# Performance work log

Hardware: AMD Instinct MI355X
Metric: run time of the kernel (lower is better)

The kernel has to match this reference:

```python
import jax, jax.numpy as jnp
import numpy as np

# ---- constants matching init_kwargs ----
N_ELEMENT = 8
N_LINES = 32
LINES_PER_ELEM = 4  # n_line_group_each_element = [4]*8
MINIBATCH = 512
SAMPLE_N = 1024
SAMPLE_CM = 0.01
PROBE_I0 = 100000.0
SIGNAL_ATT = 1.0
DET_SOLID_ANGLE_RATIO = 0.05
N_VOXEL_MB = MINIBATCH * SAMPLE_N


def setup_inputs() -> dict:
    key = jax.random.key(0)
    k1, k2, k3, k4 = jax.random.split(key, 4)
    xp = jax.random.uniform(k1, (N_ELEMENT, MINIBATCH, SAMPLE_N), dtype=jnp.float32)
    mu_probe = jax.random.uniform(k2, (N_ELEMENT,), dtype=jnp.float32)
    fl_unit = jax.random.uniform(k3, (N_LINES,), dtype=jnp.float32)
    SA_theta = jax.random.uniform(k4, (N_LINES, N_VOXEL_MB), dtype=jnp.float32)
    return {"xp": xp, "mu_probe": mu_probe, "fl_unit": fl_unit, "SA_theta": SA_theta}


def reference(xp, mu_probe, fl_unit, SA_theta):
    # xp: (E, B, N) concentration minibatch, theta==0 so rotation is skipped.
    conc = xp  # (E, B, N)

    # Probe attenuation: per-element LAC, prefix-sum along beam axis,
    # zero-padded at entry face, summed over elements.
    lac = conc * mu_probe[:, None, None]                     # (E, B, N)
    lac_acc = jnp.cumsum(lac, axis=-1)                       # (E, B, N)
    zeros_col = jnp.zeros((N_ELEMENT, MINIBATCH, 1), dtype=conc.dtype)
    lac_acc = jnp.concatenate([zeros_col, lac_acc], axis=-1) # (E, B, N+1)
    att_exponent_acc_map = jnp.sum(lac_acc, axis=0) * (SAMPLE_CM / SAMPLE_N)  # (B, N+1)

    # Fluorescence map: line l belongs to element l // LINES_PER_ELEM.
    elem_of_line = jnp.repeat(jnp.arange(N_ELEMENT), LINES_PER_ELEM)  # (L,) const
    conc_flat = conc.reshape(N_ELEMENT, N_VOXEL_MB)                   # (E, V)
    fl_map_tot = conc_flat[elem_of_line] * fl_unit[:, None]           # (L, V)

    attenuation_flat = jnp.exp(-att_exponent_acc_map[:, :-1]).reshape(N_VOXEL_MB)
    transmission_att_exponent = att_exponent_acc_map[:, -1]           # (B,)

    probe_after_att = PROBE_I0 * attenuation_flat                     # (V,)
    fl_signal = probe_after_att[None, :] * fl_map_tot * SA_theta      # (L, V)
    fl_signal = fl_signal.reshape(N_LINES, MINIBATCH, SAMPLE_N).sum(axis=-1)
    fl_signal = fl_signal * DET_SOLID_ANGLE_RATIO * SIGNAL_ATT        # (L, B)

    return fl_signal, transmission_att_exponent
```

## Files before the change

### kernel.cpp

```cpp
#include <hip/hip_runtime.h>

constexpr int NE = 8;
constexpr int NL = 32;
constexpr int MB = 512;
constexpr int SN = 1024;
constexpr float KS   = 0.01f / 1024.0f;
constexpr float I0   = 100000.0f;
constexpr float OUTS = 0.05f;

__global__ __launch_bounds__(256)
void ppm_kernel(const float* __restrict__ xp,
                const float* __restrict__ mu,
                const float* __restrict__ fl,
                const float* __restrict__ SA,
                float* __restrict__ out)
{
    const int b    = blockIdx.x;
    const int t    = threadIdx.x;
    const int lane = t & 63;
    const int wv   = t >> 6;

    __shared__ float s_wave[4];
    __shared__ float s_acc[256 * 33];
    __shared__ float s_part[256];

    const size_t sarow = (size_t)b * SN;

    float x[NE][4];
    #pragma unroll
    for (int e = 0; e < NE; ++e) {
        const float4 v = reinterpret_cast<const float4*>(
            xp + (size_t)e * (MB * SN) + sarow)[t];
        x[e][0] = v.x; x[e][1] = v.y; x[e][2] = v.z; x[e][3] = v.w;
    }

    float4 sa[16];
    #pragma unroll
    for (int l = 0; l < 16; ++l) {
        sa[l] = reinterpret_cast<const float4*>(
            SA + ((size_t)l << 19) + sarow)[t];
    }

    float a0 = 0.f, a1 = 0.f, a2 = 0.f, a3 = 0.f;
    #pragma unroll
    for (int e = 0; e < NE; ++e) {
        const float m = mu[e];
        a0 = fmaf(m, x[e][0], a0);
        a1 = fmaf(m, x[e][1], a1);
        a2 = fmaf(m, x[e][2], a2);
        a3 = fmaf(m, x[e][3], a3);
    }
    const float e1 = a0, e2 = a0 + a1, e3 = e2 + a2;
    const float T  = e3 + a3;

    float incl = T;
    #pragma unroll
    for (int d = 1; d < 64; d <<= 1) {
        const float v = __shfl_up(incl, d, 64);
        if (lane >= d) incl += v;
    }
    if (lane == 63) s_wave[wv] = incl;
    __syncthreads();

    float woff = 0.f;
    #pragma unroll
    for (int w2 = 0; w2 < 4; ++w2) woff += (w2 < wv) ? s_wave[w2] : 0.f;
    const float bex = woff + (incl - T);

    if (t == 0) {
        out[NL * MB + b] = KS * (s_wave[0] + s_wave[1] + s_wave[2] + s_wave[3]);
    }

    const float w0  = I0 * __expf(-KS * bex);
    const float w1  = I0 * __expf(-KS * (bex + e1));
    const float w2f = I0 * __expf(-KS * (bex + e2));
    const float w3  = I0 * __expf(-KS * (bex + e3));
    #pragma unroll
    for (int e = 0; e < NE; ++e) {
        x[e][0] *= w0; x[e][1] *= w1; x[e][2] *= w2f; x[e][3] *= w3;
    }

    float4 sb[16];
    #pragma unroll
    for (int l = 0; l < 16; ++l) {
        sb[l] = reinterpret_cast<const float4*>(
            SA + ((size_t)(l + 16) << 19) + sarow)[t];
    }
    #pragma unroll
    for (int l = 0; l < 16; ++l) {
        const int e = l >> 2;
        s_acc[t * 33 + l] = x[e][0] * sa[l].x + x[e][1] * sa[l].y
                          + x[e][2] * sa[l].z + x[e][3] * sa[l].w;
    }
    #pragma unroll
    for (int l = 0; l < 16; ++l) {
        const int e = 4 + (l >> 2);
        s_acc[t * 33 + 16 + l] = x[e][0] * sb[l].x + x[e][1] * sb[l].y
                               + x[e][2] * sb[l].z + x[e][3] * sb[l].w;
    }
    __syncthreads();

    {
        const int l = t & 31, g = t >> 5;
        float s = 0.f;
        #pragma unroll
        for (int j = 0; j < 32; ++j) s += s_acc[(g * 32 + j) * 33 + l];
        s_part[t] = s;
    }
    __syncthreads();

    if (t < 32) {
        float tot = 0.f;
        #pragma unroll
        for (int g2 = 0; g2 < 8; ++g2) tot += s_part[g2 * 32 + t];
        out[t * MB + b] = OUTS * fl[t] * tot;
    }
}

extern "C" void kernel_launch(void* const* d_in, const int* in_sizes, int n_in,
                              void* d_out, int out_size, void* d_ws, size_t ws_size,
                              hipStream_t stream) {
    const float* xp = (const float*)d_in[0];
    const float* mu = (const float*)d_in[1];
    const float* fl = (const float*)d_in[2];
    const float* SA = (const float*)d_in[3];
    float* out = (float*)d_out;
    ppm_kernel<<<MB, 256, 0, stream>>>(xp, mu, fl, SA, out);
}
```

Measured before the change: 19.41 us.

## Factor block-offset attenuation out of dot products and stream SA loads before the barrier

```diff
diff --git a/kernel.cpp b/kernel.cpp
--- a/kernel.cpp
+++ b/kernel.cpp
@@ -34,11 +34,10 @@
         x[e][0] = v.x; x[e][1] = v.y; x[e][2] = v.z; x[e][3] = v.w;
     }
 
-    float4 sa[16];
+    float4 A[8], B[8];
     #pragma unroll
-    for (int l = 0; l < 16; ++l) {
-        sa[l] = reinterpret_cast<const float4*>(
-            SA + ((size_t)l << 19) + sarow)[t];
+    for (int l = 0; l < 8; ++l) {
+        A[l] = reinterpret_cast<const float4*>(SA + ((size_t)l << 19) + sarow)[t];
     }
 
     float a0 = 0.f, a1 = 0.f, a2 = 0.f, a3 = 0.f;
@@ -52,6 +51,13 @@
     }
     const float e1 = a0, e2 = a0 + a1, e3 = e2 + a2;
     const float T  = e3 + a3;
+    const float l1 = __expf(-KS * e1);
+    const float l2 = __expf(-KS * e2);
+    const float l3 = __expf(-KS * e3);
+    #pragma unroll
+    for (int e = 0; e < NE; ++e) {
+        x[e][1] *= l1; x[e][2] *= l2; x[e][3] *= l3;
+    }
 
     float incl = T;
     #pragma unroll
@@ -60,44 +66,59 @@
         if (lane >= d) incl += v;
     }
     if (lane == 63) s_wave[wv] = incl;
+
+    float acc[NL];
+    #pragma unroll
+    for (int l = 0; l < 8; ++l) {
+        B[l] = reinterpret_cast<const float4*>(SA + ((size_t)(8 + l) << 19) + sarow)[t];
+    }
+    #pragma unroll
+    for (int l = 0; l < 8; ++l) {
+        const int e = l >> 2;
+        acc[l] = x[e][0] * A[l].x + x[e][1] * A[l].y
+               + x[e][2] * A[l].z + x[e][3] * A[l].w;
+    }
+    #pragma unroll
+    for (int l = 0; l < 8; ++l) {
+        A[l] = reinterpret_cast<const float4*>(SA + ((size_t)(16 + l) << 19) + sarow)[t];
+    }
+    #pragma unroll
+    for (int l = 0; l < 8; ++l) {
+        const int e = 2 + (l >> 2);
+        acc[8 + l] = x[e][0] * B[l].x + x[e][1] * B[l].y
+                   + x[e][2] * B[l].z + x[e][3] * B[l].w;
+    }
+    #pragma unroll
+    for (int l = 0; l < 8; ++l) {
+        B[l] = reinterpret_cast<const float4*>(SA + ((size_t)(24 + l) << 19) + sarow)[t];
+    }
+    #pragma unroll
+    for (int l = 0; l < 8; ++l) {
+        const int e = 4 + (l >> 2);
+        acc[16 + l] = x[e][0] * A[l].x + x[e][1] * A[l].y
+                    + x[e][2] * A[l].z + x[e][3] * A[l].w;
+    }
+    #pragma unroll
+    for (int l = 0; l < 8; ++l) {
+        const int e = 6 + (l >> 2);
+        acc[24 + l] = x[e][0] * B[l].x + x[e][1] * B[l].y
+                    + x[e][2] * B[l].z + x[e][3] * B[l].w;
+    }
+
     __syncthreads();
 
     float woff = 0.f;
     #pragma unroll
     for (int w2 = 0; w2 < 4; ++w2) woff += (w2 < wv) ? s_wave[w2] : 0.f;
     const float bex = woff + (incl - T);
+    const float W   = I0 * __expf(-KS * bex);
 
     if (t == 0) {
         out[NL * MB + b] = KS * (s_wave[0] + s_wave[1] + s_wave[2] + s_wave[3]);
     }
 
-    const float w0  = I0 * __expf(-KS * bex);
-    const float w1  = I0 * __expf(-KS * (bex + e1));
-    const float w2f = I0 * __expf(-KS * (bex + e2));
-    const float w3  = I0 * __expf(-KS * (bex + e3));
     #pragma unroll
-    for (int e = 0; e < NE; ++e) {
-        x[e][0] *= w0; x[e][1] *= w1; x[e][2] *= w2f; x[e][3] *= w3;
-    }
-
-    float4 sb[16];
-    #pragma unroll
-    for (int l = 0; l < 16; ++l) {
-        sb[l] = reinterpret_cast<const float4*>(
-            SA + ((size_t)(l + 16) << 19) + sarow)[t];
-    }
-    #pragma unroll
-    for (int l = 0; l < 16; ++l) {
-        const int e = l >> 2;
-        s_acc[t * 33 + l] = x[e][0] * sa[l].x + x[e][1] * sa[l].y
-                          + x[e][2] * sa[l].z + x[e][3] * sa[l].w;
-    }
-    #pragma unroll
-    for (int l = 0; l < 16; ++l) {
-        const int e = 4 + (l >> 2);
-        s_acc[t * 33 + 16 + l] = x[e][0] * sb[l].x + x[e][1] * sb[l].y
-                               + x[e][2] * sb[l].z + x[e][3] * sb[l].w;
-    }
+    for (int l = 0; l < NL; ++l) s_acc[t * 33 + l] = W * acc[l];
     __syncthreads();
 
     {
```

Result: slower. 20.51 us (+5.6%).

## Split each batch row across two blocks by line half

Applied to the files above, without the earlier changes.

```diff
diff --git a/kernel.cpp b/kernel.cpp
--- a/kernel.cpp
+++ b/kernel.cpp
@@ -15,13 +15,15 @@
                 const float* __restrict__ SA,
                 float* __restrict__ out)
 {
-    const int b    = blockIdx.x;
+    const int bh   = blockIdx.x;
+    const int b    = bh >> 1;
+    const int h    = bh & 1;
     const int t    = threadIdx.x;
     const int lane = t & 63;
     const int wv   = t >> 6;
 
     __shared__ float s_wave[4];
-    __shared__ float s_acc[256 * 33];
+    __shared__ float s_acc[256 * 17];
     __shared__ float s_part[256];
 
     const size_t sarow = (size_t)b * SN;
@@ -32,13 +34,6 @@
         const float4 v = reinterpret_cast<const float4*>(
             xp + (size_t)e * (MB * SN) + sarow)[t];
         x[e][0] = v.x; x[e][1] = v.y; x[e][2] = v.z; x[e][3] = v.w;
-    }
-
-    float4 sa[16];
-    #pragma unroll
-    for (int l = 0; l < 16; ++l) {
-        sa[l] = reinterpret_cast<const float4*>(
-            SA + ((size_t)l << 19) + sarow)[t];
     }
 
     float a0 = 0.f, a1 = 0.f, a2 = 0.f, a3 = 0.f;
@@ -67,7 +62,7 @@
     for (int w2 = 0; w2 < 4; ++w2) woff += (w2 < wv) ? s_wave[w2] : 0.f;
     const float bex = woff + (incl - T);
 
-    if (t == 0) {
+    if (h == 0 && t == 0) {
         out[NL * MB + b] = KS * (s_wave[0] + s_wave[1] + s_wave[2] + s_wave[3]);
     }
 
@@ -75,45 +70,42 @@
     const float w1  = I0 * __expf(-KS * (bex + e1));
     const float w2f = I0 * __expf(-KS * (bex + e2));
     const float w3  = I0 * __expf(-KS * (bex + e3));
+
+    float y[4][4];
     #pragma unroll
-    for (int e = 0; e < NE; ++e) {
-        x[e][0] *= w0; x[e][1] *= w1; x[e][2] *= w2f; x[e][3] *= w3;
+    for (int i = 0; i < 4; ++i) {
+        const int e = 4 * h + i;
+        y[i][0] = w0  * x[e][0];
+        y[i][1] = w1  * x[e][1];
+        y[i][2] = w2f * x[e][2];
+        y[i][3] = w3  * x[e][3];
     }
 
-    float4 sb[16];
     #pragma unroll
-    for (int l = 0; l < 16; ++l) {
-        sb[l] = reinterpret_cast<const float4*>(
-            SA + ((size_t)(l + 16) << 19) + sarow)[t];
-    }
-    #pragma unroll
-    for (int l = 0; l < 16; ++l) {
-        const int e = l >> 2;
-        s_acc[t * 33 + l] = x[e][0] * sa[l].x + x[e][1] * sa[l].y
-                          + x[e][2] * sa[l].z + x[e][3] * sa[l].w;
-    }
-    #pragma unroll
-    for (int l = 0; l < 16; ++l) {
-        const int e = 4 + (l >> 2);
-        s_acc[t * 33 + 16 + l] = x[e][0] * sb[l].x + x[e][1] * sb[l].y
-                               + x[e][2] * sb[l].z + x[e][3] * sb[l].w;
+    for (int i = 0; i < 16; ++i) {
+        const float4 sa = reinterpret_cast<const float4*>(
+            SA + ((size_t)(16 * h + i) << 19) + sarow)[t];
+        const int q = i >> 2;
+        s_acc[t * 17 + i] = y[q][0] * sa.x + y[q][1] * sa.y
+                          + y[q][2] * sa.z + y[q][3] * sa.w;
     }
     __syncthreads();
 
     {
-        const int l = t & 31, g = t >> 5;
+        const int l = t & 15, g = t >> 4;
         float s = 0.f;
         #pragma unroll
-        for (int j = 0; j < 32; ++j) s += s_acc[(g * 32 + j) * 33 + l];
+        for (int j = 0; j < 16; ++j) s += s_acc[(g * 16 + j) * 17 + l];
         s_part[t] = s;
     }
     __syncthreads();
 
-    if (t < 32) {
+    if (t < 16) {
         float tot = 0.f;
         #pragma unroll
-        for (int g2 = 0; g2 < 8; ++g2) tot += s_part[g2 * 32 + t];
-        out[t * MB + b] = OUTS * fl[t] * tot;
+        for (int g2 = 0; g2 < 16; ++g2) tot += s_part[g2 * 16 + t];
+        const int l = 16 * h + t;
+        out[l * MB + b] = OUTS * fl[l] * tot;
     }
 }
 
@@ -125,5 +117,5 @@
     const float* fl = (const float*)d_in[2];
     const float* SA = (const float*)d_in[3];
     float* out = (float*)d_out;
-    ppm_kernel<<<MB, 256, 0, stream>>>(xp, mu, fl, SA, out);
+    ppm_kernel<<<2 * MB, 256, 0, stream>>>(xp, mu, fl, SA, out);
 }
```

Result: slower. 22.30 us (+14.9%).
